# Kernel optimization log

Hardware: AMD Instinct MI355X
Metric: run time of the kernel (lower is better)

The kernel has to match this reference:

```python
import jax, jax.numpy as jnp
import numpy as np

N_NODES = 200000
N_EDGES = 3200000
N_GRAPHS = 64
IN_DIM, HIDDEN, OUT_DIM = 128, 16, 64


def setup_inputs() -> dict:
    key = jax.random.key(0)
    ks = jax.random.split(key, 5)
    x = jax.random.normal(ks[0], (N_NODES, IN_DIM), dtype=jnp.float32)
    edge_index = jax.random.randint(ks[1], (2, N_EDGES), 0, N_NODES, dtype=jnp.int64)
    batch = jnp.sort(jax.random.randint(ks[2], (N_NODES,), 0, N_GRAPHS, dtype=jnp.int64))
    W1 = jax.random.normal(ks[3], (IN_DIM, HIDDEN), dtype=jnp.float32) * (1.0 / np.sqrt(IN_DIM))
    W2 = jax.random.normal(ks[4], (HIDDEN, OUT_DIM), dtype=jnp.float32) * (1.0 / np.sqrt(HIDDEN))
    b1 = jnp.zeros((HIDDEN,), jnp.float32)
    b2 = jnp.zeros((OUT_DIM,), jnp.float32)
    return {"x": x, "edge_index": edge_index, "batch": batch,
            "W1": W1, "b1": b1, "W2": W2, "b2": b2, "training": 0}


def _gcn_conv(x, W, b, row, col, n_nodes):
    # PyG GCNConv: add-self-loop symmetric normalization, transform then
    # gather-from-row / scatter-add-to-col.  (row, col) already include self-loops.
    h = x @ W                                             # [N, out]
    deg = jnp.zeros((n_nodes,), h.dtype).at[col].add(1.0)  # degree incl. self-loop (>=1)
    dinv = deg ** -0.5
    norm = dinv[row] * dinv[col]                          # [E+N]
    out = jnp.zeros((n_nodes, W.shape[1]), h.dtype).at[col].add(h[row] * norm[:, None])
    return out + b


def reference(x, edge_index, batch, W1, b1, W2, b2, training):
    n = x.shape[0]
    loops = jnp.arange(n, dtype=edge_index.dtype)
    row = jnp.concatenate([edge_index[0], loops])
    col = jnp.concatenate([edge_index[1], loops])
    h = _gcn_conv(x, W1, b1, row, col, n)
    h = jax.nn.relu(h)
    # F.dropout with training=False is identity (reference is deterministic)
    h = _gcn_conv(h, W2, b2, row, col, n)
    # per-graph sum pooling: replaces the Python torch.where loop
    graph_embeds = jax.ops.segment_sum(h, batch, num_segments=N_GRAPHS)
    return graph_embeds
```

## Files before the change

### kernel.cpp

```cpp
#include <hip/hip_runtime.h>


#define TPB 256
#define CHUNK 4096
#define BK_SHIFT 10
#define NPB 1024

__device__ __forceinline__ float bf2f(unsigned short u) {
    union { unsigned int i; float f; } v; v.i = ((unsigned int)u) << 16; return v.f;
}
__device__ __forceinline__ unsigned short f2bf(float f) {
    union { float f; unsigned int i; } v; v.f = f;
    unsigned int r = v.i + 0x7fff + ((v.i >> 16) & 1);
    return (unsigned short)(r >> 16);
}

__global__ __launch_bounds__(TPB) void hist_kernel(const int* __restrict__ col,
                                                   int* __restrict__ counts,
                                                   int E, int nblk, int nbuck) {
    __shared__ int hist[256];
    int t = threadIdx.x;
    if (t < nbuck) hist[t] = 0;
    __syncthreads();
    int e0 = blockIdx.x * CHUNK;
    for (int i = t; i < CHUNK; i += TPB) {
        int e = e0 + i;
        if (e < E) atomicAdd(&hist[col[e] >> BK_SHIFT], 1);
    }
    __syncthreads();
    if (t < nbuck) counts[t * nblk + blockIdx.x] = hist[t];
}

__global__ __launch_bounds__(TPB) void scan1_kernel(const int* __restrict__ in,
                                                    int* __restrict__ out,
                                                    int* __restrict__ bsum, int L) {
    __shared__ int s[TPB];
    int t = threadIdx.x;
    int i = blockIdx.x * TPB + t;
    int d = (i < L) ? in[i] : 0;
    s[t] = d; __syncthreads();
    for (int off = 1; off < TPB; off <<= 1) {
        int v = (t >= off) ? s[t - off] : 0;
        __syncthreads();
        s[t] += v;
        __syncthreads();
    }
    if (i < L) out[i] = s[t] - d;
    if (t == TPB - 1) bsum[blockIdx.x] = s[t];
}

__global__ __launch_bounds__(1024) void scan2_kernel(int* __restrict__ bsum, int nb) {
    __shared__ int s[1024];
    int t = threadIdx.x;
    int v = (t < nb) ? bsum[t] : 0;
    s[t] = v; __syncthreads();
    for (int off = 1; off < 1024; off <<= 1) {
        int u = (t >= off) ? s[t - off] : 0;
        __syncthreads();
        s[t] += u;
        __syncthreads();
    }
    if (t < nb) bsum[t] = s[t] - v;
}

__global__ __launch_bounds__(TPB) void scan3g_kernel(int* __restrict__ out,
                                                     const int* __restrict__ bsum, int L) {
    int i = blockIdx.x * TPB + threadIdx.x;
    if (i < L) out[i] += bsum[blockIdx.x];
}

__global__ __launch_bounds__(TPB) void s1c_gemm_kernel(
        const int* __restrict__ row, const int* __restrict__ col,
        const int* __restrict__ cbase, int E, int nblk, int nbuck,
        int2* __restrict__ bucketed,
        const float* __restrict__ x, const float* __restrict__ W1,
        float* __restrict__ h1, int N, int nbg) {
    __shared__ int cur[256];
    __shared__ float w1s[128 * 16];
    int b = (int)blockIdx.x, t = threadIdx.x;
    int M = min(nblk, nbg);
    int role, id;
    if (b < 2 * M) { role = b & 1; id = b >> 1; }
    else           { role = (nblk > nbg) ? 0 : 1; id = b - M; }

    if (role == 0) {
        if (t < nbuck) cur[t] = cbase[t * nblk + id];
        __syncthreads();
        int e0 = id * CHUNK;
        for (int i = t; i < CHUNK; i += TPB) {
            int e = e0 + i;
            if (e < E) {
                int c = col[e];
                int pos = atomicAdd(&cur[c >> BK_SHIFT], 1);
                bucketed[pos] = make_int2(c, row[e]);
            }
        }
        return;
    }
    for (int i = t; i < 128 * 16; i += TPB) w1s[i] = W1[i];
    __syncthreads();
    int n = id * TPB + t;
    if (n >= N) return;
    const float4* xr = (const float4*)(x + (size_t)n * 128);
    float acc[16];
#pragma unroll
    for (int k = 0; k < 16; ++k) acc[k] = 0.f;
#pragma unroll 1
    for (int g = 0; g < 8; ++g) {
        float4 v0 = xr[g * 4 + 0], v1 = xr[g * 4 + 1];
        float4 v2 = xr[g * 4 + 2], v3 = xr[g * 4 + 3];
        float xv[16] = {v0.x, v0.y, v0.z, v0.w, v1.x, v1.y, v1.z, v1.w,
                        v2.x, v2.y, v2.z, v2.w, v3.x, v3.y, v3.z, v3.w};
#pragma unroll
        for (int cc = 0; cc < 16; ++cc) {
            const float4* w4 = (const float4*)&w1s[(g * 16 + cc) * 16];
            float4 wa = w4[0], wb = w4[1], wc = w4[2], wd = w4[3];
            float xc = xv[cc];
            acc[0]  = fmaf(xc, wa.x, acc[0]);  acc[1]  = fmaf(xc, wa.y, acc[1]);
            acc[2]  = fmaf(xc, wa.z, acc[2]);  acc[3]  = fmaf(xc, wa.w, acc[3]);
            acc[4]  = fmaf(xc, wb.x, acc[4]);  acc[5]  = fmaf(xc, wb.y, acc[5]);
            acc[6]  = fmaf(xc, wb.z, acc[6]);  acc[7]  = fmaf(xc, wb.w, acc[7]);
            acc[8]  = fmaf(xc, wc.x, acc[8]);  acc[9]  = fmaf(xc, wc.y, acc[9]);
            acc[10] = fmaf(xc, wc.z, acc[10]); acc[11] = fmaf(xc, wc.w, acc[11]);
            acc[12] = fmaf(xc, wd.x, acc[12]); acc[13] = fmaf(xc, wd.y, acc[13]);
            acc[14] = fmaf(xc, wd.z, acc[14]); acc[15] = fmaf(xc, wd.w, acc[15]);
        }
    }
    float4* o = (float4*)(h1 + (size_t)n * 16);
    o[0] = make_float4(acc[0], acc[1], acc[2], acc[3]);
    o[1] = make_float4(acc[4], acc[5], acc[6], acc[7]);
    o[2] = make_float4(acc[8], acc[9], acc[10], acc[11]);
    o[3] = make_float4(acc[12], acc[13], acc[14], acc[15]);
}

__global__ __launch_bounds__(TPB) void sort_kernel(
        const int2* __restrict__ bucketed, const int* __restrict__ cbase,
        int E, int nblk, int nbuck,
        int* __restrict__ csr, int* __restrict__ offs, float* __restrict__ dinv,
        const float* __restrict__ h1, unsigned short* __restrict__ h1p, int N) {
    __shared__ int lhist[NPB];
    __shared__ int part[TPB];
    __shared__ float sdinv[NPB];
    int bk = blockIdx.x, t = threadIdx.x;
    int n0 = bk << BK_SHIFT;
    int n1 = min(n0 + NPB, N);
    int e0 = cbase[bk * nblk];
    int e1 = (bk + 1 < nbuck) ? cbase[(bk + 1) * nblk] : E;

    for (int i = t; i < NPB; i += TPB) lhist[i] = 0;
    __syncthreads();
    for (int i = e0 + t; i < e1; i += TPB)
        atomicAdd(&lhist[bucketed[i].x & (NPB - 1)], 1);
    __syncthreads();

    int base = t * 4;
    int c0 = lhist[base], c1 = lhist[base + 1], c2 = lhist[base + 2], c3 = lhist[base + 3];
    int s = c0 + c1 + c2 + c3;
    part[t] = s;
    __syncthreads();
    for (int off = 1; off < TPB; off <<= 1) {
        int v = (t >= off) ? part[t - off] : 0;
        __syncthreads();
        part[t] += v;
        __syncthreads();
    }
    int o0 = e0 + part[t] - s;
    int o1 = o0 + c0, o2 = o1 + c1, o3 = o2 + c2;
    lhist[base] = o0; lhist[base + 1] = o1; lhist[base + 2] = o2; lhist[base + 3] = o3;
    sdinv[base]     = rsqrtf((float)c0 + 1.0f);
    sdinv[base + 1] = rsqrtf((float)c1 + 1.0f);
    sdinv[base + 2] = rsqrtf((float)c2 + 1.0f);
    sdinv[base + 3] = rsqrtf((float)c3 + 1.0f);
    int n = n0 + base;
    if (n + 0 < N) { offs[n + 0] = o0; dinv[n + 0] = sdinv[base]; }
    if (n + 1 < N) { offs[n + 1] = o1; dinv[n + 1] = sdinv[base + 1]; }
    if (n + 2 < N) { offs[n + 2] = o2; dinv[n + 2] = sdinv[base + 2]; }
    if (n + 3 < N) { offs[n + 3] = o3; dinv[n + 3] = sdinv[base + 3]; }
    __syncthreads();

    for (int i = e0 + t; i < e1; i += TPB) {
        int2 cr = bucketed[i];
        int pos = atomicAdd(&lhist[cr.x & (NPB - 1)], 1);
        csr[pos] = cr.y;
    }
    int nq = (n1 - n0) * 4;
    for (int i = t; i < nq; i += TPB) {
        float dv = sdinv[i >> 2];
        float4 v = ((const float4*)h1)[(size_t)n0 * 4 + i];
        ((ushort4*)h1p)[(size_t)n0 * 4 + i] =
            make_ushort4(f2bf(v.x * dv), f2bf(v.y * dv), f2bf(v.z * dv), f2bf(v.w * dv));
    }
    if (bk == 0 && t == 0) offs[N] = E;
}

__global__ __launch_bounds__(TPB) void gather1_kernel(const int* __restrict__ csr,
                                                      const int* __restrict__ offs,
                                                      const unsigned short* __restrict__ h1p,
                                                      const float* __restrict__ dinv,
                                                      const float* __restrict__ b1,
                                                      unsigned short* __restrict__ h2p, int N) {
    int t = threadIdx.x;
    int c = blockIdx.x * 16 + (t >> 4);
    int k = t & 15;
    if (c >= N) return;
    int p0 = offs[c], p1 = offs[c + 1];
    float acc = 0.f;
    for (int p = p0; p < p1; p += 16) {
        int idx = p + k;
        int s = csr[min(idx, p1 - 1)];
        int rem = p1 - p;
        float v[16];
#pragma unroll
        for (int j = 0; j < 16; ++j) {
            int sj = __shfl(s, j, 16);
            v[j] = bf2f(h1p[(size_t)sj * 16 + k]);
        }
#pragma unroll
        for (int j = 0; j < 16; ++j) acc += (j < rem) ? v[j] : 0.f;
    }
    float dc = dinv[c];
    float self = bf2f(h1p[(size_t)c * 16 + k]);
    float a = fmaf(dc, acc + self, b1[k]);
    h2p[(size_t)c * 16 + k] = f2bf(dc * fmaxf(a, 0.f));
}

__global__ __launch_bounds__(TPB) void gather2_kernel(const int* __restrict__ csr,
                                                      const int* __restrict__ offs,
                                                      const unsigned short* __restrict__ h2p,
                                                      const float* __restrict__ dinv,
                                                      float* __restrict__ a2, int N) {
    int t = threadIdx.x;
    int c = blockIdx.x * 16 + (t >> 4);
    int k = t & 15;
    if (c >= N) return;
    int p0 = offs[c], p1 = offs[c + 1];
    float acc = 0.f;
    for (int p = p0; p < p1; p += 16) {
        int idx = p + k;
        int s = csr[min(idx, p1 - 1)];
        int rem = p1 - p;
        float v[16];
#pragma unroll
        for (int j = 0; j < 16; ++j) {
            int sj = __shfl(s, j, 16);
            v[j] = bf2f(h2p[(size_t)sj * 16 + k]);
        }
#pragma unroll
        for (int j = 0; j < 16; ++j) acc += (j < rem) ? v[j] : 0.f;
    }
    float self = bf2f(h2p[(size_t)c * 16 + k]);
    a2[(size_t)c * 16 + k] = dinv[c] * (acc + self);
}

__global__ __launch_bounds__(TPB) void final_kernel(const float* __restrict__ a2,
                                                    const float* __restrict__ W2,
                                                    const float* __restrict__ b2,
                                                    const int* __restrict__ batch,
                                                    float* __restrict__ out, int N) {
    __shared__ float w2s[16 * 64];
    int t = threadIdx.x;
    for (int i = t; i < 16 * 64; i += TPB) w2s[i] = W2[i];
    __syncthreads();

    int wave = t >> 6, lane = t & 63;
    int n0 = blockIdx.x * 256 + wave * 64;
    float b2k = b2[lane];
    int g_cur = -1;
    float acc = 0.f;
    for (int i = 0; i < 64; ++i) {
        int n = n0 + i;
        if (n >= N) break;
        const float* ar = a2 + (size_t)n * 16;
        float val = b2k;
#pragma unroll
        for (int j = 0; j < 16; ++j) val = fmaf(ar[j], w2s[j * 64 + lane], val);
        int g = batch[n];
        if (g != g_cur) {
            if (g_cur >= 0) atomicAdd(&out[(size_t)g_cur * 64 + lane], acc);
            acc = 0.f;
            g_cur = g;
        }
        acc += val;
    }
    if (g_cur >= 0) atomicAdd(&out[(size_t)g_cur * 64 + lane], acc);
}

static inline size_t align64(size_t v) { return (v + 63) & ~(size_t)63; }

extern "C" void kernel_launch(void* const* d_in, const int* in_sizes, int n_in,
                              void* d_out, int out_size, void* d_ws, size_t ws_size,
                              hipStream_t stream) {
    const float* x     = (const float*)d_in[0];
    const int*   ei    = (const int*)d_in[1];
    const int*   batch = (const int*)d_in[2];
    const float* W1    = (const float*)d_in[3];
    const float* b1    = (const float*)d_in[4];
    const float* W2    = (const float*)d_in[5];
    const float* b2    = (const float*)d_in[6];

    const int N = in_sizes[0] / 128;
    const int E = in_sizes[1] / 2;
    const int* row = ei;
    const int* col = ei + E;

    const int NBLK  = (E + CHUNK - 1) / CHUNK;
    const int NBUCK = (N + NPB - 1) / NPB;
    const int L     = NBUCK * NBLK;
    const int NBS   = (L + TPB - 1) / TPB;
    const int NBG   = (N + TPB - 1) / TPB;

    char* p = (char*)d_ws;
    int*            counts   = (int*)p;            p += align64((size_t)L * 4);
    int*            bsum     = (int*)p;            p += align64(1024 * 4);
    int2*           bucketed = (int2*)p;           p += align64((size_t)E * 8);
    int*            csr      = (int*)p;            p += align64((size_t)E * 4);
    int*            offs     = (int*)p;            p += align64((size_t)(N + 1) * 4);
    float*          dinv     = (float*)p;          p += align64((size_t)N * 4);
    float*          h1       = (float*)p;          p += align64((size_t)N * 16 * 4);
    unsigned short* h1p      = (unsigned short*)p; p += align64((size_t)N * 16 * 2);
    unsigned short* h2p      = (unsigned short*)p; p += align64((size_t)N * 16 * 2);
    float*          a2       = h1;
    float*          out      = (float*)d_out;

    hipMemsetAsync(out, 0, (size_t)out_size * sizeof(float), stream);

    hist_kernel<<<NBLK, TPB, 0, stream>>>(col, counts, E, NBLK, NBUCK);
    scan1_kernel<<<NBS, TPB, 0, stream>>>(counts, counts, bsum, L);
    scan2_kernel<<<1, 1024, 0, stream>>>(bsum, NBS);
    scan3g_kernel<<<NBS, TPB, 0, stream>>>(counts, bsum, L);
    s1c_gemm_kernel<<<NBLK + NBG, TPB, 0, stream>>>(row, col, counts, E, NBLK, NBUCK,
                                                    bucketed, x, W1, h1, N, NBG);
    sort_kernel<<<NBUCK, TPB, 0, stream>>>(bucketed, counts, E, NBLK, NBUCK,
                                           csr, offs, dinv, h1, h1p, N);
    gather1_kernel<<<(N + 15) / 16, TPB, 0, stream>>>(csr, offs, h1p, dinv, b1, h2p, N);
    gather2_kernel<<<(N + 15) / 16, TPB, 0, stream>>>(csr, offs, h2p, dinv, a2, N);
    final_kernel<<<(N + 255) / 256, TPB, 0, stream>>>(a2, W2, b2, batch, out, N);
}
```

Baseline: 398.9 us.

## Pack bucketed edges into 32-bit words, halve bucket size, unroll gathers to 32

```diff
diff --git a/kernel.cpp b/kernel.cpp
--- a/kernel.cpp
+++ b/kernel.cpp
@@ -2,9 +2,9 @@
 
 
 #define TPB 256
-#define CHUNK 4096
-#define BK_SHIFT 10
-#define NPB 1024
+#define CHUNK 8192
+#define BK_SHIFT 9
+#define NPB 512
 
 __device__ __forceinline__ float bf2f(unsigned short u) {
     union { unsigned int i; float f; } v; v.i = ((unsigned int)u) << 16; return v.f;
@@ -18,9 +18,9 @@
 __global__ __launch_bounds__(TPB) void hist_kernel(const int* __restrict__ col,
                                                    int* __restrict__ counts,
                                                    int E, int nblk, int nbuck) {
-    __shared__ int hist[256];
-    int t = threadIdx.x;
-    if (t < nbuck) hist[t] = 0;
+    __shared__ int hist[512];
+    int t = threadIdx.x;
+    for (int i = t; i < nbuck; i += TPB) hist[i] = 0;
     __syncthreads();
     int e0 = blockIdx.x * CHUNK;
     for (int i = t; i < CHUNK; i += TPB) {
@@ -28,7 +28,7 @@
         if (e < E) atomicAdd(&hist[col[e] >> BK_SHIFT], 1);
     }
     __syncthreads();
-    if (t < nbuck) counts[t * nblk + blockIdx.x] = hist[t];
+    for (int i = t; i < nbuck; i += TPB) counts[i * nblk + blockIdx.x] = hist[i];
 }
 
 __global__ __launch_bounds__(TPB) void scan1_kernel(const int* __restrict__ in,
@@ -72,10 +72,10 @@
 __global__ __launch_bounds__(TPB) void s1c_gemm_kernel(
         const int* __restrict__ row, const int* __restrict__ col,
         const int* __restrict__ cbase, int E, int nblk, int nbuck,
-        int2* __restrict__ bucketed,
+        int* __restrict__ bucketed,
         const float* __restrict__ x, const float* __restrict__ W1,
         float* __restrict__ h1, int N, int nbg) {
-    __shared__ int cur[256];
+    __shared__ int cur[NPB];
     __shared__ float w1s[128 * 16];
     int b = (int)blockIdx.x, t = threadIdx.x;
     int M = min(nblk, nbg);
@@ -84,7 +84,7 @@
     else           { role = (nblk > nbg) ? 0 : 1; id = b - M; }
 
     if (role == 0) {
-        if (t < nbuck) cur[t] = cbase[t * nblk + id];
+        for (int i = t; i < nbuck; i += TPB) cur[i] = cbase[i * nblk + id];
         __syncthreads();
         int e0 = id * CHUNK;
         for (int i = t; i < CHUNK; i += TPB) {
@@ -92,7 +92,7 @@
             if (e < E) {
                 int c = col[e];
                 int pos = atomicAdd(&cur[c >> BK_SHIFT], 1);
-                bucketed[pos] = make_int2(c, row[e]);
+                bucketed[pos] = ((c & (NPB - 1)) << 18) | row[e];
             }
         }
         return;
@@ -134,7 +134,7 @@
 }
 
 __global__ __launch_bounds__(TPB) void sort_kernel(
-        const int2* __restrict__ bucketed, const int* __restrict__ cbase,
+        const int* __restrict__ bucketed, const int* __restrict__ cbase,
         int E, int nblk, int nbuck,
         int* __restrict__ csr, int* __restrict__ offs, float* __restrict__ dinv,
         const float* __restrict__ h1, unsigned short* __restrict__ h1p, int N) {
@@ -147,15 +147,15 @@
     int e0 = cbase[bk * nblk];
     int e1 = (bk + 1 < nbuck) ? cbase[(bk + 1) * nblk] : E;
 
-    for (int i = t; i < NPB; i += TPB) lhist[i] = 0;
+    lhist[t] = 0; lhist[t + TPB] = 0;
     __syncthreads();
     for (int i = e0 + t; i < e1; i += TPB)
-        atomicAdd(&lhist[bucketed[i].x & (NPB - 1)], 1);
-    __syncthreads();
-
-    int base = t * 4;
-    int c0 = lhist[base], c1 = lhist[base + 1], c2 = lhist[base + 2], c3 = lhist[base + 3];
-    int s = c0 + c1 + c2 + c3;
+        atomicAdd(&lhist[bucketed[i] >> 18], 1);
+    __syncthreads();
+
+    int base = t * 2;
+    int c0 = lhist[base], c1 = lhist[base + 1];
+    int s = c0 + c1;
     part[t] = s;
     __syncthreads();
     for (int off = 1; off < TPB; off <<= 1) {
@@ -165,23 +165,19 @@
         __syncthreads();
     }
     int o0 = e0 + part[t] - s;
-    int o1 = o0 + c0, o2 = o1 + c1, o3 = o2 + c2;
-    lhist[base] = o0; lhist[base + 1] = o1; lhist[base + 2] = o2; lhist[base + 3] = o3;
+    int o1 = o0 + c0;
+    lhist[base] = o0; lhist[base + 1] = o1;
     sdinv[base]     = rsqrtf((float)c0 + 1.0f);
     sdinv[base + 1] = rsqrtf((float)c1 + 1.0f);
-    sdinv[base + 2] = rsqrtf((float)c2 + 1.0f);
-    sdinv[base + 3] = rsqrtf((float)c3 + 1.0f);
     int n = n0 + base;
     if (n + 0 < N) { offs[n + 0] = o0; dinv[n + 0] = sdinv[base]; }
     if (n + 1 < N) { offs[n + 1] = o1; dinv[n + 1] = sdinv[base + 1]; }
-    if (n + 2 < N) { offs[n + 2] = o2; dinv[n + 2] = sdinv[base + 2]; }
-    if (n + 3 < N) { offs[n + 3] = o3; dinv[n + 3] = sdinv[base + 3]; }
     __syncthreads();
 
     for (int i = e0 + t; i < e1; i += TPB) {
-        int2 cr = bucketed[i];
-        int pos = atomicAdd(&lhist[cr.x & (NPB - 1)], 1);
-        csr[pos] = cr.y;
+        int v = bucketed[i];
+        int pos = atomicAdd(&lhist[v >> 18], 1);
+        csr[pos] = v & 0x3FFFF;
     }
     int nq = (n1 - n0) * 4;
     for (int i = t; i < nq; i += TPB) {
@@ -205,18 +201,23 @@
     if (c >= N) return;
     int p0 = offs[c], p1 = offs[c + 1];
     float acc = 0.f;
-    for (int p = p0; p < p1; p += 16) {
-        int idx = p + k;
-        int s = csr[min(idx, p1 - 1)];
+    for (int p = p0; p < p1; p += 32) {
+        int s0 = csr[min(p + k, p1 - 1)];
+        int s1 = csr[min(p + 16 + k, p1 - 1)];
         int rem = p1 - p;
-        float v[16];
+        float v[32];
 #pragma unroll
         for (int j = 0; j < 16; ++j) {
-            int sj = __shfl(s, j, 16);
+            int sj = __shfl(s0, j, 16);
             v[j] = bf2f(h1p[(size_t)sj * 16 + k]);
         }
 #pragma unroll
-        for (int j = 0; j < 16; ++j) acc += (j < rem) ? v[j] : 0.f;
+        for (int j = 0; j < 16; ++j) {
+            int sj = __shfl(s1, j, 16);
+            v[16 + j] = bf2f(h1p[(size_t)sj * 16 + k]);
+        }
+#pragma unroll
+        for (int j = 0; j < 32; ++j) acc += (j < rem) ? v[j] : 0.f;
     }
     float dc = dinv[c];
     float self = bf2f(h1p[(size_t)c * 16 + k]);
@@ -235,18 +236,23 @@
     if (c >= N) return;
     int p0 = offs[c], p1 = offs[c + 1];
     float acc = 0.f;
-    for (int p = p0; p < p1; p += 16) {
-        int idx = p + k;
-        int s = csr[min(idx, p1 - 1)];
+    for (int p = p0; p < p1; p += 32) {
+        int s0 = csr[min(p + k, p1 - 1)];
+        int s1 = csr[min(p + 16 + k, p1 - 1)];
         int rem = p1 - p;
-        float v[16];
+        float v[32];
 #pragma unroll
         for (int j = 0; j < 16; ++j) {
-            int sj = __shfl(s, j, 16);
+            int sj = __shfl(s0, j, 16);
             v[j] = bf2f(h2p[(size_t)sj * 16 + k]);
         }
 #pragma unroll
-        for (int j = 0; j < 16; ++j) acc += (j < rem) ? v[j] : 0.f;
+        for (int j = 0; j < 16; ++j) {
+            int sj = __shfl(s1, j, 16);
+            v[16 + j] = bf2f(h2p[(size_t)sj * 16 + k]);
+        }
+#pragma unroll
+        for (int j = 0; j < 32; ++j) acc += (j < rem) ? v[j] : 0.f;
     }
     float self = bf2f(h2p[(size_t)c * 16 + k]);
     a2[(size_t)c * 16 + k] = dinv[c] * (acc + self);
@@ -312,7 +318,7 @@
     char* p = (char*)d_ws;
     int*            counts   = (int*)p;            p += align64((size_t)L * 4);
     int*            bsum     = (int*)p;            p += align64(1024 * 4);
-    int2*           bucketed = (int2*)p;           p += align64((size_t)E * 8);
+    int*            bucketed = (int*)p;            p += align64((size_t)E * 4);
     int*            csr      = (int*)p;            p += align64((size_t)E * 4);
     int*            offs     = (int*)p;            p += align64((size_t)(N + 1) * 4);
     float*          dinv     = (float*)p;          p += align64((size_t)N * 4);
```

Result: no change. 397.2 us (-0.4%).
